# Kernel optimization log

Hardware: AMD Instinct MI355X
Metric: run time of the kernel (lower is better)

## Reference

```python
import jax, jax.numpy as jnp
import numpy as np

S, B, D, H, MLP_H, W = 2048, 4, 1024, 16, 4096, 16
EPS = 1e-6

def _ln(x):
    m = jnp.mean(x, axis=-1, keepdims=True)
    v = jnp.var(x, axis=-1, keepdims=True)
    return (x - m) / jnp.sqrt(v + EPS)

def setup_inputs() -> dict:
    key = jax.random.key(0)
    ks = jax.random.split(key, 12)
    sc = lambda k, shape, fan: jax.random.normal(k, shape, jnp.float32) / np.sqrt(fan)
    return {
        'x': jax.random.normal(ks[0], (S, B, D), jnp.float32),
        'c': jax.random.normal(ks[1], (B, D), jnp.float32),
        'ada_w': sc(ks[2], (6 * D, D), D),
        'ada_b': jax.random.normal(ks[3], (6 * D,), jnp.float32) * 0.02,
        'in_proj_w': sc(ks[4], (3 * D, D), D),
        'in_proj_b': jax.random.normal(ks[5], (3 * D,), jnp.float32) * 0.02,
        'out_proj_w': sc(ks[6], (D, D), D),
        'out_proj_b': jax.random.normal(ks[7], (D,), jnp.float32) * 0.02,
        'mlp_w1': sc(ks[8], (MLP_H, D), D),
        'mlp_b1': jax.random.normal(ks[9], (MLP_H,), jnp.float32) * 0.02,
        'mlp_w2': sc(ks[10], (D, MLP_H), MLP_H),
        'mlp_b2': jax.random.normal(ks[11], (D,), jnp.float32) * 0.02,
        'num_heads': H,
        'window_size': W,
    }

def _attn(x, in_proj_w, in_proj_b, out_proj_w, out_proj_b, num_heads, window_size):
    s, b, d = x.shape
    dh = d // num_heads
    qkv = x @ in_proj_w.T + in_proj_b            # [S,B,3D]
    q, k, v = jnp.split(qkv, 3, axis=-1)
    def heads(t):  # [S,B,D] -> [B,H,S,dh]
        return t.reshape(s, b, num_heads, dh).transpose(1, 2, 0, 3)
    q, k, v = heads(q), heads(k), heads(v)
    scores = jnp.einsum('bhsd,bhtd->bhst', q, k) / np.sqrt(dh)
    idx = jnp.arange(s)
    band = jnp.abs(idx[:, None] - idx[None, :]) <= window_size  # [S,S]
    scores = jnp.where(band[None, None], scores, -jnp.inf)
    attn = jax.nn.softmax(scores, axis=-1)
    o = jnp.einsum('bhst,bhtd->bhsd', attn, v)   # [B,H,S,dh]
    o = o.transpose(2, 0, 1, 3).reshape(s, b, d)
    return o @ out_proj_w.T + out_proj_b

def reference(x, c, ada_w, ada_b, in_proj_w, in_proj_b, out_proj_w, out_proj_b, mlp_w1, mlp_b1, mlp_w2, mlp_b2, num_heads, window_size):
    mod = jax.nn.relu(c) @ ada_w.T + ada_b       # [B,6D]
    sh_msa, sc_msa, g_msa, sh_mlp, sc_mlp, g_mlp = jnp.split(mod, 6, axis=1)
    xm = _ln(x) * (1.0 + sc_msa[None]) + sh_msa[None]
    x = x + g_msa[None] * _attn(xm, in_proj_w, in_proj_b, out_proj_w, out_proj_b, num_heads, window_size)
    xm = _ln(x) * (1.0 + sc_mlp[None]) + sh_mlp[None]
    h = jax.nn.relu(xm @ mlp_w1.T + mlp_b1)
    mlp_out = h @ mlp_w2.T + mlp_b2
    return x + g_mlp[None] * mlp_out
```

## Files before the change

kernel.cpp:

```cpp
#include <hip/hip_runtime.h>

#define S_LEN 2048
#define BATCH 4
#define DMODEL 1024
#define NHEAD 16
#define MROWS (S_LEN * BATCH)
#define MOD6 (6 * DMODEL)

typedef float f32x4 __attribute__((ext_vector_type(4)));
typedef short bf16x8 __attribute__((ext_vector_type(8)));
typedef unsigned short ushort_t;

__device__ __forceinline__ unsigned short f2bf(float f) {
  unsigned u = __float_as_uint(f);
  u += 0x7FFF + ((u >> 16) & 1);
  return (unsigned short)(u >> 16);
}
__device__ __forceinline__ float bf2f(unsigned short h) {
  return __uint_as_float(((unsigned)h) << 16);
}
__device__ __forceinline__ float wave_sum(float v) {
#pragma unroll
  for (int off = 32; off > 0; off >>= 1) v += __shfl_xor(v, off, 64);
  return v;
}
__device__ __forceinline__ void mfma16(f32x4& c, bf16x8 a, bf16x8 b) {
  asm volatile("v_mfma_f32_16x16x32_bf16 %0, %1, %2, %0" : "+v"(c) : "v"(a), "v"(b));
}
__device__ __forceinline__ void mfma_fence() {
  __builtin_amdgcn_sched_barrier(0);
  asm volatile("s_nop 7\n\ts_nop 7\n\ts_nop 7");
  __builtin_amdgcn_sched_barrier(0);
}
__device__ __forceinline__ void async16(const void* g, void* l) {
  __builtin_amdgcn_global_load_lds((const __attribute__((address_space(1))) void*)g,
                                   (__attribute__((address_space(3))) void*)l, 16, 0, 0);
}

__launch_bounds__(256)
__global__ void castk(const float4* __restrict__ in, ushort4* __restrict__ out, int n4) {
  int i = blockIdx.x * 256 + threadIdx.x;
  if (i < n4) {
    float4 v = in[i];
    ushort4 o;
    o.x = f2bf(v.x); o.y = f2bf(v.y); o.z = f2bf(v.z); o.w = f2bf(v.w);
    out[i] = o;
  }
}

__launch_bounds__(256)
__global__ void ada_k(const float* __restrict__ c, const float* __restrict__ aw,
                      const float* __restrict__ ab, float* __restrict__ mod) {
  int j = blockIdx.x;
  int b = threadIdx.x >> 6;
  int l = threadIdx.x & 63;
  const float* wrow = aw + (size_t)j * DMODEL;
  const float* crow = c + b * DMODEL;
  float s = 0.f;
#pragma unroll 4
  for (int i = l; i < DMODEL; i += 64) {
    float cv = crow[i];
    cv = cv > 0.f ? cv : 0.f;
    s += cv * wrow[i];
  }
  s = wave_sum(s);
  if (l == 0) mod[b * MOD6 + j] = s + ab[j];
}

__launch_bounds__(256)
__global__ void ln_mod(const float* __restrict__ x, const float* __restrict__ mod,
                       int sh_off, int sc_off, ushort_t* __restrict__ out) {
  __shared__ float red[8];
  int row = blockIdx.x;
  int b = row & 3;
  int tid = threadIdx.x;
  const float4* xr = (const float4*)(x + (size_t)row * DMODEL);
  float4 v = xr[tid];
  float s = v.x + v.y + v.z + v.w;
  float s2 = v.x * v.x + v.y * v.y + v.z * v.z + v.w * v.w;
  s = wave_sum(s);
  s2 = wave_sum(s2);
  int w = tid >> 6, l = tid & 63;
  if (l == 0) { red[w] = s; red[4 + w] = s2; }
  __syncthreads();
  s = red[0] + red[1] + red[2] + red[3];
  s2 = red[4] + red[5] + red[6] + red[7];
  float mean = s * (1.0f / DMODEL);
  float var = s2 * (1.0f / DMODEL) - mean * mean;
  float inv = rsqrtf(var + 1e-6f);
  const float* shp = mod + b * MOD6 + sh_off;
  const float* scp = mod + b * MOD6 + sc_off;
  float vv[4] = {v.x, v.y, v.z, v.w};
  ushort4 ov;
  ushort_t* op = (ushort_t*)&ov;
#pragma unroll
  for (int j = 0; j < 4; j++) {
    int idx = tid * 4 + j;
    float y = (vv[j] - mean) * inv * (1.0f + scp[idx]) + shp[idx];
    op[j] = f2bf(y);
  }
  ((ushort4*)(out + (size_t)row * DMODEL))[tid] = ov;
}

__launch_bounds__(256)
__global__ void attn_mfma(const ushort_t* __restrict__ qkv, ushort_t* __restrict__ out) {
  const int l = threadIdx.x & 63;
  const int widx = blockIdx.x * 4 + (threadIdx.x >> 6);
  const int qblk = widx & 63;
  const int bh = widx >> 6;
  const int h = bh & 15;
  const int b = bh >> 4;
  const int q0 = qblk * 32;
  int k0 = q0 - 16;
  if (k0 < 0) k0 = 0;
  if (k0 > S_LEN - 64) k0 = S_LEN - 64;
  const int lr = l & 15;
  const int g = l >> 4;

  const char* base = (const char*)qkv;

  bf16x8 qf[2][2], kf[4][2];
#pragma unroll
  for (int nt = 0; nt < 2; nt++) {
    size_t rowb = (size_t)((q0 + 16 * nt + lr) * 4 + b) * 6144 + h * 128 + 16 * g;
#pragma unroll
    for (int ks = 0; ks < 2; ks++)
      qf[nt][ks] = *(const bf16x8*)(base + rowb + 64 * ks);
  }
#pragma unroll
  for (int mt = 0; mt < 4; mt++) {
    size_t rowb = (size_t)((k0 + 16 * mt + lr) * 4 + b) * 6144 + 2048 + h * 128 + 16 * g;
#pragma unroll
    for (int ks = 0; ks < 2; ks++)
      kf[mt][ks] = *(const bf16x8*)(base + rowb + 64 * ks);
  }

  f32x4 acc[4][2] = {};
  __builtin_amdgcn_s_setprio(1);
#pragma unroll
  for (int mt = 0; mt < 4; mt++)
#pragma unroll
    for (int nt = 0; nt < 2; nt++)
#pragma unroll
      for (int ks = 0; ks < 2; ks++)
        mfma16(acc[mt][nt], kf[mt][ks], qf[nt][ks]);
  __builtin_amdgcn_s_setprio(0);
  mfma_fence();

  float p0[16], p1[16];
  const int sq0 = q0 + lr, sq1 = q0 + 16 + lr;
  float m0 = -1e30f, m1 = -1e30f;
#pragma unroll
  for (int mt = 0; mt < 4; mt++)
#pragma unroll
    for (int i = 0; i < 4; i++) {
      int sk = k0 + 16 * mt + 4 * g + i;
      int d0 = sq0 - sk, d1 = sq1 - sk;
      float s0 = (d0 <= 16 && d0 >= -16) ? acc[mt][0][i] * 0.125f : -1e30f;
      float s1 = (d1 <= 16 && d1 >= -16) ? acc[mt][1][i] * 0.125f : -1e30f;
      p0[mt * 4 + i] = s0;
      p1[mt * 4 + i] = s1;
      m0 = fmaxf(m0, s0);
      m1 = fmaxf(m1, s1);
    }
  m0 = fmaxf(m0, __shfl_xor(m0, 16, 64));
  m0 = fmaxf(m0, __shfl_xor(m0, 32, 64));
  m1 = fmaxf(m1, __shfl_xor(m1, 16, 64));
  m1 = fmaxf(m1, __shfl_xor(m1, 32, 64));
  float l0 = 0.f, l1 = 0.f;
#pragma unroll
  for (int j = 0; j < 16; j++) {
    float e0 = __expf(p0[j] - m0);
    float e1 = __expf(p1[j] - m1);
    p0[j] = e0; p1[j] = e1;
    l0 += e0; l1 += e1;
  }
  l0 += __shfl_xor(l0, 16, 64); l0 += __shfl_xor(l0, 32, 64);
  l1 += __shfl_xor(l1, 16, 64); l1 += __shfl_xor(l1, 32, 64);
  const float inv0 = 1.0f / l0, inv1 = 1.0f / l1;

  const size_t vb = (size_t)b * 6144 + 4096 + h * 128;
  for (int c = 0; c < 8; c++) {
    float o0[8] = {}, o1[8] = {};
#pragma unroll
    for (int mt = 0; mt < 4; mt++)
#pragma unroll
      for (int i = 0; i < 4; i++) {
        int t = k0 + 16 * mt + 4 * g + i;
        bf16x8 v = *(const bf16x8*)(base + (size_t)t * 24576 + vb + 16 * c);
        float pa = p0[mt * 4 + i], pb = p1[mt * 4 + i];
#pragma unroll
        for (int d = 0; d < 8; d++) {
          float vf = bf2f((unsigned short)v[d]);
          o0[d] += pa * vf;
          o1[d] += pb * vf;
        }
      }
#pragma unroll
    for (int d = 0; d < 8; d++) {
      o0[d] += __shfl_xor(o0[d], 16, 64); o0[d] += __shfl_xor(o0[d], 32, 64);
      o1[d] += __shfl_xor(o1[d], 16, 64); o1[d] += __shfl_xor(o1[d], 32, 64);
    }
    if (g < 2) {
      int sq = q0 + 16 * g + lr;
      bf16x8 ov;
#pragma unroll
      for (int d = 0; d < 8; d++) {
        float val = (g ? o1[d] : o0[d]) * (g ? inv1 : inv0);
        ov[d] = (short)f2bf(val);
      }
      *(bf16x8*)((char*)out + (size_t)(sq * 4 + b) * 2048 + h * 128 + c * 16) = ov;
    }
  }
}

template <int EPI, int K>
__launch_bounds__(256, 4)
__global__ void gemm_bt(const ushort_t* __restrict__ A, const ushort_t* __restrict__ W,
                        const float* __restrict__ bias, const float* __restrict__ res,
                        const float* __restrict__ gmod, void* __restrict__ outp,
                        int M, int N) {
  __shared__ alignas(16) ushort_t As[128 * 64];
  __shared__ alignas(16) ushort_t Bs[128 * 64];
  const int tid = threadIdx.x;
  const int w = tid >> 6;
  const int l = tid & 63;

  int bx = blockIdx.x, by = blockIdx.y;
  {
    const int nbx = gridDim.x;
    const int nwg = nbx * gridDim.y;
    if ((nwg & 7) == 0) {
      int lin = by * nbx + bx;
      int nlin = (lin & 7) * (nwg >> 3) + (lin >> 3);
      bx = nlin % nbx;
      by = nlin / nbx;
    }
  }
  const int row0 = by * 128;
  const int col0 = bx * 128;
  const int wr = (w >> 1) * 64;
  const int wc = (w & 1) * 64;

  f32x4 acc[4][4] = {};

  const int srow = tid >> 3;
  const int scc = (((tid & 7) ^ (srow & 7)) << 3);
  const ushort_t* ga = A + (size_t)(row0 + srow) * K + scc;
  const ushort_t* gb = W + (size_t)(col0 + srow) * K + scc;
  char* lA = (char*)As + w * 1024;
  char* lB = (char*)Bs + w * 1024;

  const int lrow = l & 15;
  const int g = l >> 4;
  const int cx0 = ((g ^ (lrow & 7)) << 4);
  const int cx1 = (((4 + g) ^ (lrow & 7)) << 4);
  const int arow = (wr + lrow) * 128;
  const int brow = (wc + lrow) * 128;

  const int nk = K >> 6;
  for (int it = 0; it < nk; ++it) {
#pragma unroll
    for (int r = 0; r < 4; r++) async16(ga + (size_t)(32 * r) * K, lA + r * 4096);
#pragma unroll
    for (int r = 0; r < 4; r++) async16(gb + (size_t)(32 * r) * K, lB + r * 4096);
    ga += 64;
    gb += 64;
    __syncthreads();
#pragma unroll
    for (int kk = 0; kk < 2; kk++) {
      const int cx = kk ? cx1 : cx0;
      bf16x8 afr[4], bfr[4];
#pragma unroll
      for (int m = 0; m < 4; m++) afr[m] = *(const bf16x8*)((char*)As + arow + m * 2048 + cx);
#pragma unroll
      for (int n = 0; n < 4; n++) bfr[n] = *(const bf16x8*)((char*)Bs + brow + n * 2048 + cx);
#pragma unroll
      for (int m = 0; m < 4; m++)
#pragma unroll
        for (int n = 0; n < 4; n++) mfma16(acc[m][n], afr[m], bfr[n]);
    }
    __syncthreads();
  }
  mfma_fence();

  const int crow = row0 + wr + g * 4;
  const int ccol = col0 + wc + lrow;
#pragma unroll
  for (int m = 0; m < 4; m++) {
#pragma unroll
    for (int i = 0; i < 4; i++) {
      int grow = crow + m * 16 + i;
#pragma unroll
      for (int n = 0; n < 4; n++) {
        int gcol = ccol + n * 16;
        float v = acc[m][n][i] + bias[gcol];
        if constexpr (EPI == 0) {
          ((ushort_t*)outp)[(size_t)grow * N + gcol] = f2bf(v);
        } else if constexpr (EPI == 1) {
          ((ushort_t*)outp)[(size_t)grow * N + gcol] = f2bf(v > 0.f ? v : 0.f);
        } else {
          int bb = grow & 3;
          ((float*)outp)[(size_t)grow * N + gcol] =
              res[(size_t)grow * N + gcol] + gmod[bb * MOD6 + gcol] * v;
        }
      }
    }
  }
}

extern "C" void kernel_launch(void* const* d_in, const int* in_sizes, int n_in,
                              void* d_out, int out_size, void* d_ws, size_t ws_size,
                              hipStream_t stream) {
  const float* x     = (const float*)d_in[0];
  const float* c     = (const float*)d_in[1];
  const float* ada_w = (const float*)d_in[2];
  const float* ada_b = (const float*)d_in[3];
  const float* in_w  = (const float*)d_in[4];
  const float* in_b  = (const float*)d_in[5];
  const float* out_w = (const float*)d_in[6];
  const float* out_b = (const float*)d_in[7];
  const float* w1    = (const float*)d_in[8];
  const float* b1    = (const float*)d_in[9];
  const float* w2    = (const float*)d_in[10];
  const float* b2    = (const float*)d_in[11];

  char* ws = (char*)d_ws;
  float* mod    = (float*)ws;
  ushort_t* wq  = (ushort_t*)(ws + 98304);
  ushort_t* wo  = (ushort_t*)(ws + 6389760);
  ushort_t* wm1 = (ushort_t*)(ws + 8486912);
  ushort_t* wm2 = (ushort_t*)(ws + 16875520);
  ushort_t* xm  = (ushort_t*)(ws + 25264128);
  ushort_t* qkv = (ushort_t*)(ws + 42041344);
  ushort_t* att = (ushort_t*)(ws + 92372992);
  ushort_t* h   = (ushort_t*)(ws + 42041344);
  float* x1 = (float*)d_out;

  castk<<<(3072 * 1024 / 4 + 255) / 256, 256, 0, stream>>>((const float4*)in_w, (ushort4*)wq, 3072 * 1024 / 4);
  castk<<<(1024 * 1024 / 4 + 255) / 256, 256, 0, stream>>>((const float4*)out_w, (ushort4*)wo, 1024 * 1024 / 4);
  castk<<<(4096 * 1024 / 4 + 255) / 256, 256, 0, stream>>>((const float4*)w1, (ushort4*)wm1, 4096 * 1024 / 4);
  castk<<<(1024 * 4096 / 4 + 255) / 256, 256, 0, stream>>>((const float4*)w2, (ushort4*)wm2, 1024 * 4096 / 4);

  ada_k<<<MOD6, 256, 0, stream>>>(c, ada_w, ada_b, mod);

  ln_mod<<<MROWS, 256, 0, stream>>>(x, mod, 0, 1024, xm);
  gemm_bt<0, 1024><<<dim3(3072 / 128, MROWS / 128), 256, 0, stream>>>(xm, wq, in_b, nullptr, nullptr, qkv, MROWS, 3072);
  attn_mfma<<<(BATCH * NHEAD * (S_LEN / 32)) / 4, 256, 0, stream>>>(qkv, att);
  gemm_bt<2, 1024><<<dim3(1024 / 128, MROWS / 128), 256, 0, stream>>>(att, wo, out_b, x, mod + 2 * DMODEL, x1, MROWS, 1024);
  ln_mod<<<MROWS, 256, 0, stream>>>(x1, mod, 3 * DMODEL, 4 * DMODEL, xm);
  gemm_bt<1, 1024><<<dim3(4096 / 128, MROWS / 128), 256, 0, stream>>>(xm, wm1, b1, nullptr, nullptr, h, MROWS, 4096);
  gemm_bt<2, 4096><<<dim3(1024 / 128, MROWS / 128), 256, 0, stream>>>(h, wm2, b2, x1, mod + 5 * DMODEL, (float*)d_out, MROWS, 1024);
}
```

Before: 323.2 us.

## Double-buffer LDS tiles in GEMM to overlap async loads with MFMA

Gives the bf16 GEMM two LDS buffers for the A and B tiles and prefetches the next K-tile with async loads while the current tile is consumed by MFMAs. Explicit vmcnt waits and raw barriers replace the per-iteration __syncthreads pair. It also raises wave priority around the MFMA block and lowers launch bounds to 2 blocks per CU, since LDS use doubles to 64KB per block. The aim is to hide global-load latency, at the cost of lower occupancy.

New measurement: 334.6 us. 1.04x slower.

```diff
diff --git a/kernel.cpp b/kernel.cpp
--- a/kernel.cpp
+++ b/kernel.cpp
@@ -215,13 +215,13 @@
 }
 
 template <int EPI, int K>
-__launch_bounds__(256, 4)
+__launch_bounds__(256, 2)
 __global__ void gemm_bt(const ushort_t* __restrict__ A, const ushort_t* __restrict__ W,
                         const float* __restrict__ bias, const float* __restrict__ res,
                         const float* __restrict__ gmod, void* __restrict__ outp,
                         int M, int N) {
-  __shared__ alignas(16) ushort_t As[128 * 64];
-  __shared__ alignas(16) ushort_t Bs[128 * 64];
+  __shared__ alignas(16) ushort_t As[2][128 * 64];
+  __shared__ alignas(16) ushort_t Bs[2][128 * 64];
   const int tid = threadIdx.x;
   const int w = tid >> 6;
   const int l = tid & 63;
@@ -248,8 +248,7 @@
   const int scc = (((tid & 7) ^ (srow & 7)) << 3);
   const ushort_t* ga = A + (size_t)(row0 + srow) * K + scc;
   const ushort_t* gb = W + (size_t)(col0 + srow) * K + scc;
-  char* lA = (char*)As + w * 1024;
-  char* lB = (char*)Bs + w * 1024;
+  const int ldst = w * 1024;
 
   const int lrow = l & 15;
   const int g = l >> 4;
@@ -259,28 +258,55 @@
   const int brow = (wc + lrow) * 128;
 
   const int nk = K >> 6;
-  for (int it = 0; it < nk; ++it) {
+  {
+    char* lA = (char*)As[0] + ldst;
+    char* lB = (char*)Bs[0] + ldst;
 #pragma unroll
     for (int r = 0; r < 4; r++) async16(ga + (size_t)(32 * r) * K, lA + r * 4096);
 #pragma unroll
     for (int r = 0; r < 4; r++) async16(gb + (size_t)(32 * r) * K, lB + r * 4096);
     ga += 64;
     gb += 64;
-    __syncthreads();
+  }
+  int cur = 0;
+  for (int it = 0; it < nk; ++it) {
+    if (it + 1 < nk) {
+      char* lA = (char*)As[cur ^ 1] + ldst;
+      char* lB = (char*)Bs[cur ^ 1] + ldst;
+#pragma unroll
+      for (int r = 0; r < 4; r++) async16(ga + (size_t)(32 * r) * K, lA + r * 4096);
+#pragma unroll
+      for (int r = 0; r < 4; r++) async16(gb + (size_t)(32 * r) * K, lB + r * 4096);
+      ga += 64;
+      gb += 64;
+      asm volatile("s_waitcnt vmcnt(8)" ::: "memory");
+    } else {
+      asm volatile("s_waitcnt vmcnt(0)" ::: "memory");
+    }
+    __builtin_amdgcn_sched_barrier(0);
+    __builtin_amdgcn_s_barrier();
+    __builtin_amdgcn_sched_barrier(0);
+    const char* Ab = (const char*)As[cur];
+    const char* Bb = (const char*)Bs[cur];
 #pragma unroll
     for (int kk = 0; kk < 2; kk++) {
       const int cx = kk ? cx1 : cx0;
       bf16x8 afr[4], bfr[4];
 #pragma unroll
-      for (int m = 0; m < 4; m++) afr[m] = *(const bf16x8*)((char*)As + arow + m * 2048 + cx);
-#pragma unroll
-      for (int n = 0; n < 4; n++) bfr[n] = *(const bf16x8*)((char*)Bs + brow + n * 2048 + cx);
+      for (int m = 0; m < 4; m++) afr[m] = *(const bf16x8*)(Ab + arow + m * 2048 + cx);
+#pragma unroll
+      for (int n = 0; n < 4; n++) bfr[n] = *(const bf16x8*)(Bb + brow + n * 2048 + cx);
+      __builtin_amdgcn_s_setprio(1);
 #pragma unroll
       for (int m = 0; m < 4; m++)
 #pragma unroll
         for (int n = 0; n < 4; n++) mfma16(acc[m][n], afr[m], bfr[n]);
-    }
-    __syncthreads();
+      __builtin_amdgcn_s_setprio(0);
+    }
+    __builtin_amdgcn_sched_barrier(0);
+    __builtin_amdgcn_s_barrier();
+    __builtin_amdgcn_sched_barrier(0);
+    cur ^= 1;
   }
   mfma_fence();
 
```
